# Optimization experiments

Hardware: AMD Instinct MI355X
Metric: run time of the kernel (lower is better)

Reference implementation:

```python
import jax, jax.numpy as jnp
import numpy as np

LATDIM = 128
ANCHOR_SET_NUM = 64
N_NODES = 10000

def setup_inputs() -> dict:
    key = jax.random.key(0)
    k1, k2, k3, k4, k5 = jax.random.split(key, 5)
    embeds = jax.random.normal(k1, (N_NODES, LATDIM), dtype=jnp.float32)
    dists_array = jax.random.uniform(k2, (ANCHOR_SET_NUM, N_NODES), dtype=jnp.float32)
    W_hidden = jax.random.normal(k3, (LATDIM, 2 * LATDIM), dtype=jnp.float32) * 0.05
    b_hidden = jax.random.normal(k4, (LATDIM,), dtype=jnp.float32) * 0.05
    anchorset_id = jax.random.randint(k5, (ANCHOR_SET_NUM,), 0, N_NODES, dtype=jnp.int64 if jax.config.jax_enable_x64 else jnp.int32)
    return {"embeds": embeds, "dists_array": dists_array, "W_hidden": W_hidden,
            "b_hidden": b_hidden, "anchorset_id": anchorset_id}

def reference(embeds, dists_array, W_hidden, b_hidden, anchorset_id):
    A, N = dists_array.shape
    d = embeds.shape[1]
    set_ids_emb = embeds[anchorset_id]                       # [A, d] anchor gather
    # messages[i, j] = set_ids_emb[j] * dists[j, i]
    messages = set_ids_emb[None, :, :] * dists_array.T[:, :, None]   # [N, A, d]
    # faithful to torch: embeds.repeat(A,1).reshape(-1, A, d) -> embeds[(i*A+j) % N]
    self_feature = jnp.tile(embeds, (A, 1)).reshape(N, A, d)          # [N, A, d]
    m = jnp.concatenate([messages, self_feature], axis=-1)            # [N, A, 2d]
    h = jnp.einsum('nak,ok->nao', m, W_hidden) + b_hidden             # [N, A, d]
    return jnp.mean(h, axis=1)                                        # [N, d]
```

## Files before the change

kernel.cpp:

```cpp
#include <hip/hip_runtime.h>

#define LATDIM 128
#define ANUM   64
#define NNODES 10000
#define PERIOD 625
#define TN     16
#define ABLK   64
#define SBLK   625


__global__ __launch_bounds__(256) void prep_kernel(
    const float* __restrict__ embeds,
    const float* __restrict__ W,
    const float* __restrict__ b,
    const int*   __restrict__ anchor,
    float* __restrict__ P,
    float* __restrict__ T2b)
{
    __shared__ float X_s[LATDIM];
    __shared__ float R_s[LATDIM];
    __shared__ float Xp[8][LATDIM];
    const int tid = threadIdx.x;
    const float4* X_s4 = (const float4*)X_s;

    if (blockIdx.x < ABLK) {
        const int a = blockIdx.x;
        if (tid < 32) {
            ((float4*)X_s)[tid] =
                *((const float4*)(embeds + (size_t)anchor[a] * LATDIM) + tid);
        }
        __syncthreads();

        const int o = tid & 127;
        const int h = tid >> 7;
        const float4* Wr = (const float4*)(W + (size_t)o * (2 * LATDIM) + h * 64);
        float acc = 0.f;
        #pragma unroll
        for (int k4 = 0; k4 < 16; ++k4) {
            float4 w4 = Wr[k4];
            float4 x4 = X_s4[h * 16 + k4];
            acc += w4.x * x4.x + w4.y * x4.y + w4.z * x4.z + w4.w * x4.w;
        }
        if (h == 1) R_s[o] = acc;
        __syncthreads();
        if (h == 0) P[(size_t)a * LATDIM + o] = acc + R_s[o];
    } else {
        const int s = blockIdx.x - ABLK;
        const int row0 = (64 * s) % NNODES;

        const int c4 = tid & 31;
        const int hg = tid >> 5;
        float4 sum = {0.f, 0.f, 0.f, 0.f};
        #pragma unroll
        for (int i = 0; i < 8; ++i) {
            int row = row0 + 8 * i + hg;
            if (row >= NNODES) row -= NNODES;
            float4 v = *((const float4*)(embeds + (size_t)row * LATDIM) + c4);
            sum.x += v.x; sum.y += v.y; sum.z += v.z; sum.w += v.w;
        }
        ((float4*)&Xp[hg][0])[c4] = sum;
        __syncthreads();
        if (tid < LATDIM) {
            float t = Xp[0][tid];
            #pragma unroll
            for (int g = 1; g < 8; ++g) t += Xp[g][tid];
            X_s[tid] = t;
        }
        __syncthreads();

        const int o = tid & 127;
        const int h = tid >> 7;
        const float4* Wr =
            (const float4*)(W + (size_t)o * (2 * LATDIM) + LATDIM + h * 64);
        float acc = 0.f;
        #pragma unroll
        for (int k4 = 0; k4 < 16; ++k4) {
            float4 w4 = Wr[k4];
            float4 x4 = X_s4[h * 16 + k4];
            acc += w4.x * x4.x + w4.y * x4.y + w4.z * x4.z + w4.w * x4.w;
        }
        if (h == 1) R_s[o] = acc;
        __syncthreads();
        if (h == 0)
            T2b[(size_t)s * LATDIM + o] =
                b[o] + (acc + R_s[o]) * (1.0f / ANUM);
    }
}

__global__ __launch_bounds__(256) void main_kernel(
    const float* __restrict__ dists,
    const float* __restrict__ P,
    const float* __restrict__ T2b,
    float* __restrict__ out)
{
    __shared__ float P_s[ANUM * LATDIM];
    const int tid = threadIdx.x;

    {
        float4* P_s4 = (float4*)P_s;
        const float4* Pg = (const float4*)P;
        #pragma unroll
        for (int it = 0; it < (ANUM * LATDIM / 4) / 256; ++it)
            P_s4[it * 256 + tid] = Pg[it * 256 + tid];
    }
    __syncthreads();

    const int lane = tid & 63;
    const int w    = __builtin_amdgcn_readfirstlane(tid >> 6);
    const int o    = (w & 1) * 64 + lane;
    const int nc   = w >> 1;
    const int nb   = blockIdx.x * TN + nc * 8;

    float acc[8] = {};
    #pragma unroll 4
    for (int a = 0; a < ANUM; ++a) {
        const float p = P_s[a * LATDIM + o];
        const float* __restrict__ drow = dists + (size_t)a * NNODES + nb;
        #pragma unroll
        for (int j = 0; j < 8; ++j)
            acc[j] += drow[j] * p;
    }

    #pragma unroll
    for (int j = 0; j < 8; ++j) {
        const int n = nb + j;
        const int s = n % PERIOD;
        out[(size_t)n * LATDIM + o] =
            acc[j] * (1.0f / ANUM) + T2b[(size_t)s * LATDIM + o];
    }
}

extern "C" void kernel_launch(void* const* d_in, const int* in_sizes, int n_in,
                              void* d_out, int out_size, void* d_ws, size_t ws_size,
                              hipStream_t stream) {
    const float* embeds = (const float*)d_in[0];
    const float* dists  = (const float*)d_in[1];
    const float* W      = (const float*)d_in[2];
    const float* b      = (const float*)d_in[3];
    const int*   anchor = (const int*)d_in[4];
    float* out = (float*)d_out;

    float* P   = (float*)d_ws;
    float* T2b = P + ANUM * LATDIM;

    prep_kernel<<<ABLK + SBLK, 256, 0, stream>>>(embeds, W, b, anchor, P, T2b);
    main_kernel<<<NNODES / TN, 256, 0, stream>>>(dists, P, T2b, out);
}
```

Measured before the change: 82.37 us.

## Halve per-block node tile, drop LDS staging of P, remap blocks across XCDs

The main kernel now handles 8 nodes per block instead of 16, which doubles the grid to 1250 blocks. P is read directly from global memory (through cache) instead of being staged into 32KB of shared memory. Block IDs are remapped so that consecutive node tiles land on the same XCD, which should improve L2 locality for dists rows. The aim is more occupancy and no LDS prologue, at the cost of more redundant P reads per block and smaller per-thread work.

```diff
diff --git a/kernel.cpp b/kernel.cpp
--- a/kernel.cpp
+++ b/kernel.cpp
@@ -4,9 +4,9 @@
 #define ANUM   64
 #define NNODES 10000
 #define PERIOD 625
-#define TN     16
+#define TN     8
+#define NB2    1250
 #define ABLK   64
-#define SBLK   625
 
 
 __global__ __launch_bounds__(256) void prep_kernel(
@@ -39,7 +39,7 @@
         for (int k4 = 0; k4 < 16; ++k4) {
             float4 w4 = Wr[k4];
             float4 x4 = X_s4[h * 16 + k4];
-            acc += w4.x * x4.x + w4.y * x4.y + w4.z * x4.z + w4.w * x4.w;
+            acc += w4.x*x4.x + w4.y*x4.y + w4.z*x4.z + w4.w*x4.w;
         }
         if (h == 1) R_s[o] = acc;
         __syncthreads();
@@ -77,7 +77,7 @@
         for (int k4 = 0; k4 < 16; ++k4) {
             float4 w4 = Wr[k4];
             float4 x4 = X_s4[h * 16 + k4];
-            acc += w4.x * x4.x + w4.y * x4.y + w4.z * x4.z + w4.w * x4.w;
+            acc += w4.x*x4.x + w4.y*x4.y + w4.z*x4.z + w4.w*x4.w;
         }
         if (h == 1) R_s[o] = acc;
         __syncthreads();
@@ -93,36 +93,32 @@
     const float* __restrict__ T2b,
     float* __restrict__ out)
 {
-    __shared__ float P_s[ANUM * LATDIM];
     const int tid = threadIdx.x;
-
-    {
-        float4* P_s4 = (float4*)P_s;
-        const float4* Pg = (const float4*)P;
-        #pragma unroll
-        for (int it = 0; it < (ANUM * LATDIM / 4) / 256; ++it)
-            P_s4[it * 256 + tid] = Pg[it * 256 + tid];
-    }
-    __syncthreads();
+    const int orig = blockIdx.x;
+    const int xcd = orig & 7, ii = orig >> 3;
+    const int u = (xcd < 2) ? (xcd * 157 + ii)
+                            : (314 + (xcd - 2) * 156 + ii);
 
     const int lane = tid & 63;
     const int w    = __builtin_amdgcn_readfirstlane(tid >> 6);
     const int o    = (w & 1) * 64 + lane;
     const int nc   = w >> 1;
-    const int nb   = blockIdx.x * TN + nc * 8;
+    const int nb   = u * TN + nc * 4;
 
-    float acc[8] = {};
-    #pragma unroll 4
+    const float* __restrict__ Pcol = P + o;
+    float acc[4] = {};
+    #pragma unroll 8
     for (int a = 0; a < ANUM; ++a) {
-        const float p = P_s[a * LATDIM + o];
+        const float p = Pcol[(size_t)a * LATDIM];
         const float* __restrict__ drow = dists + (size_t)a * NNODES + nb;
-        #pragma unroll
-        for (int j = 0; j < 8; ++j)
-            acc[j] += drow[j] * p;
+        acc[0] += drow[0] * p;
+        acc[1] += drow[1] * p;
+        acc[2] += drow[2] * p;
+        acc[3] += drow[3] * p;
     }
 
     #pragma unroll
-    for (int j = 0; j < 8; ++j) {
+    for (int j = 0; j < 4; ++j) {
         const int n = nb + j;
         const int s = n % PERIOD;
         out[(size_t)n * LATDIM + o] =
@@ -143,6 +139,6 @@
     float* P   = (float*)d_ws;
     float* T2b = P + ANUM * LATDIM;
 
-    prep_kernel<<<ABLK + SBLK, 256, 0, stream>>>(embeds, W, b, anchor, P, T2b);
-    main_kernel<<<NNODES / TN, 256, 0, stream>>>(dists, P, T2b, out);
+    prep_kernel<<<ABLK + PERIOD, 256, 0, stream>>>(embeds, W, b, anchor, P, T2b);
+    main_kernel<<<NB2, 256, 0, stream>>>(dists, P, T2b, out);
 }
```

Measured after the change: 80.64 us. 2.1% less time.
